# Performance work log

Measured on AMD Instinct MI355X. Metric: run time of the kernel, lower is better.

The kernel has to match this reference:

```python
import jax, jax.numpy as jnp
import numpy as np
from jax import lax

D_MODEL=1024; D_STATE=128; D_CONV=4; EXPAND=2; HEADDIM=64
D_INNER=EXPAND*D_MODEL; NHEADS=D_INNER//HEADDIM
POOL=64; SUMDIM=256; TAU1=0.5; TAU2=0.4

def rmsnorm(x, w, eps):
    return x * lax.rsqrt(jnp.mean(x*x, axis=-1, keepdims=True) + eps) * w

def silu(x):
    return x * jax.nn.sigmoid(x)

def setup_inputs():
    key = jax.random.key(0)
    ks = jax.random.split(key, 20)
    B, T = 4, 2048
    d_in_proj = 2*D_INNER + 2*D_STATE + NHEADS
    inp = {
        'x': jax.random.normal(ks[0], (B, T, D_MODEL), jnp.float32),
        'pool': jnp.zeros((B, POOL, SUMDIM), jnp.float32),
        'priorities': jnp.zeros((B, POOL), jnp.float32),
        'counts': jnp.zeros((B,), jnp.int32),
        'norm_w': jnp.ones((D_MODEL,), jnp.float32),
        'in_w': jax.random.normal(ks[1], (d_in_proj, D_MODEL), jnp.float32)*0.02,
        'conv_w': jax.random.normal(ks[2], (D_INNER+2*D_STATE, 1, D_CONV), jnp.float32)*0.1,
        'conv_b': jnp.zeros((D_INNER+2*D_STATE,), jnp.float32),
        'dt_bias': jax.random.uniform(ks[3], (NHEADS,), jnp.float32, -5.0, -1.0),
        'A_log': jnp.log(jax.random.uniform(ks[4], (NHEADS,), jnp.float32, 1.0, 16.0)),
        'Dp': jax.random.normal(ks[5], (NHEADS,), jnp.float32)*0.1 + 1.0,
        'ssm_norm_w': jnp.ones((D_INNER,), jnp.float32),
        'out_w': jax.random.normal(ks[6], (D_MODEL, D_INNER), jnp.float32)*0.02,
        'score_w1': jax.random.normal(ks[7], (D_MODEL//4, D_MODEL), jnp.float32)*0.03,
        'score_w2': jax.random.normal(ks[8], (1, D_MODEL//4), jnp.float32)*0.06,
        'summ_w': jax.random.normal(ks[9], (SUMDIM, D_MODEL), jnp.float32)*0.03,
        'q_w': jax.random.normal(ks[10], (SUMDIM, D_MODEL), jnp.float32)*0.03,
        'k_w': jax.random.normal(ks[11], (SUMDIM, SUMDIM), jnp.float32)*0.06,
        'v_w': jax.random.normal(ks[12], (D_MODEL, SUMDIM), jnp.float32)*0.06,
        'gate_w': jax.random.normal(ks[13], (D_MODEL, 2*D_MODEL), jnp.float32)*0.02,
    }
    return inp

def mamba2(u, in_w, conv_w, conv_b, dt_bias, A_log, Dp, ssm_norm_w, out_w):
    B, T, _ = u.shape
    zxbcdt = u @ in_w.T                      # [B,T,2*d_inner+2*d_state+nheads]
    z = zxbcdt[..., :D_INNER]
    xBC = zxbcdt[..., D_INNER:2*D_INNER+2*D_STATE]
    dt = jax.nn.softplus(zxbcdt[..., 2*D_INNER+2*D_STATE:] + dt_bias)  # [B,T,H]
    # causal depthwise conv over time
    xc = jnp.transpose(xBC, (0, 2, 1))       # [B,C,T]
    xc = lax.conv_general_dilated(xc, conv_w, (1,), [(D_CONV-1, 0)],
                                  dimension_numbers=('NCH', 'OIH', 'NCH'),
                                  feature_group_count=D_INNER+2*D_STATE)
    xBC = silu(jnp.transpose(xc + conv_b[None, :, None], (0, 2, 1)))
    xh = xBC[..., :D_INNER].reshape(B, T, NHEADS, HEADDIM)
    Bm = xBC[..., D_INNER:D_INNER+D_STATE]   # [B,T,N]
    Cm = xBC[..., D_INNER+D_STATE:]          # [B,T,N]
    A = -jnp.exp(A_log)                      # [H]
    dA = jnp.exp(dt * A)                     # [B,T,H]
    def step(h, inp):
        dA_t, dt_t, x_t, B_t, C_t = inp      # [B,H],[B,H],[B,H,P],[B,N],[B,N]
        h = dA_t[:, :, None, None]*h + (dt_t[:, :, None]*x_t)[..., None]*B_t[:, None, None, :]
        y = jnp.einsum('bhpn,bn->bhp', h, C_t)
        return h, y
    h0 = jnp.zeros((B, NHEADS, HEADDIM, D_STATE), u.dtype)
    xs = (jnp.swapaxes(dA, 0, 1), jnp.swapaxes(dt, 0, 1), jnp.swapaxes(xh, 0, 1),
          jnp.swapaxes(Bm, 0, 1), jnp.swapaxes(Cm, 0, 1))
    _, ys = lax.scan(step, h0, xs)           # [T,B,H,P]
    y = jnp.swapaxes(ys, 0, 1) + Dp[None, None, :, None]*xh
    y = y.reshape(B, T, D_INNER)
    y = rmsnorm(y * silu(z), ssm_norm_w, 1e-5)
    return y @ out_w.T

def pool_update(tokens, scores, pool, priorities, counts,
                summ_w):
    B, T, D = tokens.shape
    mask = scores > TAU1
    order = jnp.argsort(-scores, axis=1)     # descending
    s_scores = jnp.take_along_axis(scores, order, 1)
    s_tokens = jnp.take_along_axis(tokens, order[..., None], 1)
    s_mask = jnp.take_along_axis(mask, order, 1)
    summaries = s_tokens @ summ_w.T          # [B,T,SUMDIM]
    nslots = min(T, POOL)
    bidx = jnp.arange(B)
    def slot_step(carry, inp):
        pool, pri, counts = carry
        has_imp, imp, summ = inp             # [B],[B],[B,SUMDIM]
        add = has_imp & (counts < POOL)
        widx = jnp.minimum(counts, POOL-1)
        pool = pool.at[bidx, widx].set(jnp.where(add[:, None], summ, pool[bidx, widx]))
        pri = pri.at[bidx, widx].set(jnp.where(add, imp, pri[bidx, widx]))
        counts = counts + add.astype(counts.dtype)
        replace = has_imp & (counts >= POOL)
        min_idx = jnp.argmin(pri, axis=1)
        min_p = pri[bidx, min_idx]
        should = replace & (imp > min_p)
        pool = pool.at[bidx, min_idx].set(jnp.where(should[:, None], summ, pool[bidx, min_idx]))
        pri = pri.at[bidx, min_idx].set(jnp.where(should, imp, pri[bidx, min_idx]))
        return (pool, pri, counts), None
    xs = (jnp.swapaxes(s_mask[:, :nslots], 0, 1),
          jnp.swapaxes(s_scores[:, :nslots], 0, 1),
          jnp.swapaxes(summaries[:, :nslots], 0, 1))
    (pool, priorities, counts), _ = lax.scan(slot_step, (pool, priorities, counts), xs)
    return pool, priorities, counts

def reference(x, pool, priorities, counts, norm_w, in_w, conv_w, conv_b, dt_bias,
              A_log, Dp, ssm_norm_w, out_w, score_w1, score_w2, summ_w,
              q_w, k_w, v_w, gate_w):
    B = x.shape[0]
    y = x + mamba2(rmsnorm(x, norm_w, 1e-4), in_w, conv_w, conv_b, dt_bias,
                   A_log, Dp, ssm_norm_w, out_w)
    scores = jax.nn.sigmoid(jnp.maximum(y @ score_w1.T, 0.0) @ score_w2.T)[..., 0]
    # layer_idx % cross_layer_frequency == 0 -> update path taken
    pool, priorities, counts = pool_update(y, scores, pool, priorities, counts, summ_w)
    mask = jnp.arange(POOL)[None, :] < counts[:, None]
    q = y @ q_w.T                            # [B,T,S]
    k = pool @ k_w.T                         # [B,P,S]
    v = pool @ v_w.T                         # [B,P,D]
    attn = jnp.einsum('bts,bps->btp', q, k) / (SUMDIM ** 0.5)
    attn = jnp.where(mask[:, None, :], attn, -jnp.inf)
    attn = jnp.nan_to_num(jax.nn.softmax(attn, axis=-1), nan=0.0)
    retrieved = jnp.einsum('btp,bpd->btd', attn, v)
    gate = jax.nn.sigmoid(jnp.concatenate([y, retrieved], axis=-1) @ gate_w.T)
    rmask = ((jnp.mean(scores, axis=1) > TAU2) & (counts > 0)).astype(y.dtype)[:, None, None]
    y = y + gate * retrieved * rmask
    return (y, pool, priorities, counts)
```

## Files before the change

### kernel.cpp

```cpp
#include <hip/hip_runtime.h>


using u16 = unsigned short;
using bf16x8 = __attribute__((ext_vector_type(8))) short;
using f32x4  = __attribute__((ext_vector_type(4))) float;

#define DEV __device__ __forceinline__

#define GLOAD4(g, l)  __builtin_amdgcn_global_load_lds((const __attribute__((address_space(1))) void*)(g), (__attribute__((address_space(3))) void*)(l), 4, 0, 0)
#define GLOAD16(g, l) __builtin_amdgcn_global_load_lds((const __attribute__((address_space(1))) void*)(g), (__attribute__((address_space(3))) void*)(l), 16, 0, 0)
#define VMWAIT(N) asm volatile("s_waitcnt vmcnt(" #N ")" ::: "memory")

static constexpr int Bb = 4, T = 2048, D = 1024;
static constexpr int DIN = 2048, DST = 128, NH = 32;
static constexpr int DPROJ = 4384;
static constexpr int CCH = 2304;
static constexpr int ROWS = Bb * T;
static constexpr int NC = 4, CL = 512;

DEV float bf2f(u16 h) { union { unsigned int u; float f; } v; v.u = ((unsigned int)h) << 16; return v.f; }
DEV u16 f2bf(float f) { union { float f; unsigned int u; } v; v.f = f; unsigned int r = v.u + 0x7fffu + ((v.u >> 16) & 1u); return (u16)(r >> 16); }
DEV double sigd(double x) { return 1.0 / (1.0 + exp(-x)); }

__global__ void diag_kernel(float* o, float v) { if (threadIdx.x == 0) o[0] = v; }
__global__ void zerod_kernel(double* p, int n) { if ((int)threadIdx.x < n) p[threadIdx.x] = 0.0; }

__global__ void split3_kernel(const float* __restrict__ in, u16* __restrict__ out, long n) {
    long i = (long)blockIdx.x * 256 + threadIdx.x;
    if (i >= n) return;
    float v = in[i];
    u16 h = f2bf(v);
    float r1 = v - bf2f(h);
    u16 m = f2bf(r1);
    out[i] = h;
    out[n + i] = m;
    out[2 * n + i] = f2bf(r1 - bf2f(m));
}

__global__ __launch_bounds__(256) void rms_x_kernel(const float* __restrict__ x, const float* __restrict__ w,
                                                    u16* __restrict__ up, long pstride) {
    long row = blockIdx.x; int tid = threadIdx.x;
    const float* xr = x + row * D;
    float4 xv = *(const float4*)(xr + tid * 4);
    double ss = (double)xv.x * xv.x + (double)xv.y * xv.y + (double)xv.z * xv.z + (double)xv.w * xv.w;
    for (int off = 1; off < 64; off <<= 1) ss += __shfl_xor(ss, off);
    __shared__ double tmp[4];
    if ((tid & 63) == 0) tmp[tid >> 6] = ss;
    __syncthreads();
    double tot = tmp[0] + tmp[1] + tmp[2] + tmp[3];
    double scale = 1.0 / sqrt(tot / (double)D + 1e-4);
    float4 wv = *(const float4*)(w + tid * 4);
    long base = row * D + tid * 4;
    float vals[4];
    vals[0] = (float)((double)xv.x * scale * (double)wv.x);
    vals[1] = (float)((double)xv.y * scale * (double)wv.y);
    vals[2] = (float)((double)xv.z * scale * (double)wv.z);
    vals[3] = (float)((double)xv.w * scale * (double)wv.w);
#pragma unroll
    for (int j = 0; j < 4; j++) {
        float f = vals[j];
        u16 h = f2bf(f);
        float r1 = f - bf2f(h);
        u16 m = f2bf(r1);
        up[base + j] = h;
        up[pstride + base + j] = m;
        up[2 * pstride + base + j] = f2bf(r1 - bf2f(m));
    }
}

template <int NP>
DEV void stage_one(u16* s0, u16* s1, u16* s2, const float* __restrict__ src, long ld,
                   int row0, int lastrow, int k0, int tid) {
    int r = tid >> 1, c0 = (tid & 1) << 4;
    long rg = row0 + r; if (rg > lastrow) rg = lastrow;
    const float* p = src + rg * ld + k0 + c0;
    int base = r * 32 + c0;
    u16 h16[16], m16[16], l16[16];
#pragma unroll
    for (int q = 0; q < 4; q++) {
        float4 v4 = *(const float4*)(p + q * 4);
        float vv[4] = { v4.x, v4.y, v4.z, v4.w };
#pragma unroll
        for (int j = 0; j < 4; j++) {
            float xv = vv[j];
            u16 h = f2bf(xv);
            h16[q * 4 + j] = h;
            if constexpr (NP == 3) {
                float r1 = xv - bf2f(h);
                u16 m = f2bf(r1);
                m16[q * 4 + j] = m;
                l16[q * 4 + j] = f2bf(r1 - bf2f(m));
            }
        }
    }
    *(uint4*)(s0 + base)     = *(const uint4*)(h16);
    *(uint4*)(s0 + base + 8) = *(const uint4*)(h16 + 8);
    if constexpr (NP == 3) {
        *(uint4*)(s1 + base)     = *(const uint4*)(m16);
        *(uint4*)(s1 + base + 8) = *(const uint4*)(m16 + 8);
        *(uint4*)(s2 + base)     = *(const uint4*)(l16);
        *(uint4*)(s2 + base + 8) = *(const uint4*)(l16 + 8);
    }
}

DEV void stage_pre_dma(u16* dst, const u16* __restrict__ src, long ld,
                       int row0, int lastrow, int k0, int wid, int lane) {
#pragma unroll
    for (int j = 0; j < 2; j++) {
        int chunk = wid * 128 + j * 64 + lane;
        int r = chunk >> 2, cs = chunk & 3;
        long rg = row0 + r; if (rg > lastrow) rg = lastrow;
        const u16* g = src + rg * ld + k0 + cs * 8;
        GLOAD16(g, dst + (wid * 128 + j * 64) * 8);
    }
}

template <int NP, int MODE, bool BP, bool AP>
__global__ __launch_bounds__(256) void gemm_f32(
    const float* __restrict__ A, long lda,
    const u16* __restrict__ Ap, size_t astride,
    const float* __restrict__ B, long ldb,
    const u16* __restrict__ Bp, size_t bstride,
    int M, int N, int K,
    float* __restrict__ out0, float* __restrict__ out1,
    const float* __restrict__ aux0, const float* __restrict__ aux1,
    float* __restrict__ dtb, float* __restrict__ dab) {
    __shared__ __align__(16) u16 sm[NP * 2 * 4096];
    u16* As[3]; u16* Bs[3];
#pragma unroll
    for (int p = 0; p < NP; p++) { As[p] = sm + p * 4096; Bs[p] = sm + (NP + p) * 4096; }
    int tid = threadIdx.x, lane = tid & 63, wid = tid >> 6;
    int wr = wid >> 1, wc = wid & 1;
    int nwg = gridDim.x * gridDim.y;
    int wg = blockIdx.y * gridDim.x + blockIdx.x;
    int lin = (wg & 7) * (nwg >> 3) + (wg >> 3);
    int tM = (lin / gridDim.x) * 128, tN = (lin % gridDim.x) * 128;

    f32x4 acc[4][4];
#pragma unroll
    for (int i = 0; i < 4; i++)
#pragma unroll
        for (int j = 0; j < 4; j++) acc[i][j] = f32x4{0.f, 0.f, 0.f, 0.f};

    int nsteps = K / 32;
    for (int kt = 0; kt < nsteps; ++kt) {
        int k0 = kt * 32;
        __syncthreads();
        if constexpr (BP) {
#pragma unroll
            for (int p = 0; p < NP; p++)
                stage_pre_dma(Bs[p], Bp + (size_t)p * bstride, K, tN, N - 1, k0, wid, lane);
        }
        if constexpr (AP) {
#pragma unroll
            for (int p = 0; p < NP; p++)
                stage_pre_dma(As[p], Ap + (size_t)p * astride, K, tM, M - 1, k0, wid, lane);
        } else {
            stage_one<NP>(As[0], NP == 3 ? As[1] : nullptr, NP == 3 ? As[2] : nullptr, A, lda, tM, M - 1, k0, tid);
        }
        if constexpr (!BP) {
            stage_one<NP>(Bs[0], NP == 3 ? Bs[1] : nullptr, NP == 3 ? Bs[2] : nullptr, B, ldb, tN, N - 1, k0, tid);
        }
        __syncthreads();
        int rA = wr * 64 + (lane & 15);
        int rB = wc * 64 + (lane & 15);
        int kk = (lane >> 4) * 8;
        bf16x8 af[NP][4], bfr[NP][4];
#pragma unroll
        for (int p = 0; p < NP; p++)
#pragma unroll
            for (int i = 0; i < 4; i++) {
                af[p][i]  = *(const bf16x8*)(As[p] + (rA + i * 16) * 32 + kk);
                bfr[p][i] = *(const bf16x8*)(Bs[p] + (rB + i * 16) * 32 + kk);
            }
#pragma unroll
        for (int mi = 0; mi < 4; mi++)
#pragma unroll
            for (int ni = 0; ni < 4; ni++) {
                acc[mi][ni] = __builtin_amdgcn_mfma_f32_16x16x32_bf16(af[0][mi], bfr[0][ni], acc[mi][ni], 0, 0, 0);
                if constexpr (NP == 3) {
                    acc[mi][ni] = __builtin_amdgcn_mfma_f32_16x16x32_bf16(af[0][mi], bfr[1][ni], acc[mi][ni], 0, 0, 0);
                    acc[mi][ni] = __builtin_amdgcn_mfma_f32_16x16x32_bf16(af[1][mi], bfr[0][ni], acc[mi][ni], 0, 0, 0);
                    acc[mi][ni] = __builtin_amdgcn_mfma_f32_16x16x32_bf16(af[0][mi], bfr[2][ni], acc[mi][ni], 0, 0, 0);
                    acc[mi][ni] = __builtin_amdgcn_mfma_f32_16x16x32_bf16(af[1][mi], bfr[1][ni], acc[mi][ni], 0, 0, 0);
                    acc[mi][ni] = __builtin_amdgcn_mfma_f32_16x16x32_bf16(af[2][mi], bfr[0][ni], acc[mi][ni], 0, 0, 0);
                }
            }
    }
    int laneh = lane >> 4, lanel = lane & 15;
#pragma unroll
    for (int mi = 0; mi < 4; mi++)
#pragma unroll
        for (int ni = 0; ni < 4; ni++) {
            int col = tN + wc * 64 + ni * 16 + lanel;
            if (col >= N) continue;
#pragma unroll
            for (int r = 0; r < 4; r++) {
                long row = tM + wr * 64 + mi * 16 + laneh * 4 + r;
                float v = acc[mi][ni][r];
                if constexpr (MODE == 0) {
                    if (col < 2048) out0[row * 2048 + col] = v;
                    else if (col < 4352) out1[row * 2304 + (col - 2048)] = v;
                    else {
                        int h = col - 4352;
                        double xx = (double)v + (double)aux0[h];
                        double sp = (xx > 30.0) ? xx : log1p(exp(xx));
                        double a = -exp((double)aux1[h]);
                        dtb[row * NH + h] = (float)sp;
                        dab[row * NH + h] = (float)exp(sp * a);
                    }
                } else if constexpr (MODE == 1) {
                    out0[row * 256 + col] = fmaxf(v, 0.f);
                } else if constexpr (MODE == 2) {
                    float y = aux0[row * 1024 + col] + v;
                    out0[row * 1024 + col] = y;
                    out1[row * 2048 + col] = y;
                } else if constexpr (MODE == 3) {
                    out0[row * 256 + col] = v;
                } else {
                    double g = sigd((double)v);
                    float retr = aux0[row * 2048 + 1024 + col];
                    out0[row * 1024 + col] += (float)(g * (double)retr * (double)aux1[row >> 11]);
                }
            }
        }
}

__global__ __launch_bounds__(256) void conv_kernel(const float* __restrict__ xin, const float* __restrict__ cw,
                                                   const float* __restrict__ cb, float* __restrict__ xbc) {
    int blk = blockIdx.x;
    int ct = blk % 36; int tt = (blk / 36) % 32; int b = blk / (36 * 32);
    int c0 = ct * 64, t0 = tt * 64;
    int tid = threadIdx.x;
    __shared__ float tile[67 * 64];
    for (int i = tid; i < 67 * 64; i += 256) {
        int r = i >> 6, c = i & 63;
        int t = t0 - 3 + r;
        tile[i] = (t >= 0) ? xin[((long)(b * T + t)) * CCH + c0 + c] : 0.f;
    }
    __syncthreads();
    int c = tid & 63; int rb = (tid >> 6) * 16;
    int gc = c0 + c;
    double w0 = cw[gc * 4], w1 = cw[gc * 4 + 1], w2 = cw[gc * 4 + 2], w3 = cw[gc * 4 + 3];
    double bias = cb[gc];
    for (int j = 0; j < 16; j++) {
        int tl = rb + j;
        double a = bias + w0 * (double)tile[tl * 64 + c] + w1 * (double)tile[(tl + 1) * 64 + c]
                        + w2 * (double)tile[(tl + 2) * 64 + c] + w3 * (double)tile[(tl + 3) * 64 + c];
        xbc[((long)(b * T + t0 + tl)) * CCH + gc] = (float)(a * sigd(a));
    }
}

#define SCAN_STEP(tt) do { \
    int slot_ = (tt) & 7; \
    float dtv_ = sdt[(tt)], dav_ = sda[(tt)]; \
    float xt0_ = sx[slot_][pp], xt1_ = sx[slot_][pp + 8]; \
    float dtx0_ = dtv_ * xt0_, dtx1_ = dtv_ * xt1_; \
    const float4* BP_ = (const float4*)&sbc[slot_][0]; \
    float y0a_ = 0.f, y0b_ = 0.f, y1a_ = 0.f, y1b_ = 0.f; \
    _Pragma("unroll") \
    for (int r_ = 0; r_ < 4; r_++) { \
        float4 bv_ = BP_[r_ * 8 + sub]; \
        float4 cv_ = BP_[32 + r_ * 8 + sub]; \
        hs0[r_*4+0] = fmaf(dav_, hs0[r_*4+0], dtx0_ * bv_.x); y0a_ = fmaf(hs0[r_*4+0], cv_.x, y0a_); \
        hs0[r_*4+1] = fmaf(dav_, hs0[r_*4+1], dtx0_ * bv_.y); y0b_ = fmaf(hs0[r_*4+1], cv_.y, y0b_); \
        hs0[r_*4+2] = fmaf(dav_, hs0[r_*4+2], dtx0_ * bv_.z); y0a_ = fmaf(hs0[r_*4+2], cv_.z, y0a_); \
        hs0[r_*4+3] = fmaf(dav_, hs0[r_*4+3], dtx0_ * bv_.w); y0b_ = fmaf(hs0[r_*4+3], cv_.w, y0b_); \
        hs1[r_*4+0] = fmaf(dav_, hs1[r_*4+0], dtx1_ * bv_.x); y1a_ = fmaf(hs1[r_*4+0], cv_.x, y1a_); \
        hs1[r_*4+1] = fmaf(dav_, hs1[r_*4+1], dtx1_ * bv_.y); y1b_ = fmaf(hs1[r_*4+1], cv_.y, y1b_); \
        hs1[r_*4+2] = fmaf(dav_, hs1[r_*4+2], dtx1_ * bv_.z); y1a_ = fmaf(hs1[r_*4+2], cv_.z, y1a_); \
        hs1[r_*4+3] = fmaf(dav_, hs1[r_*4+3], dtx1_ * bv_.w); y1b_ = fmaf(hs1[r_*4+3], cv_.w, y1b_); \
    } \
    float y0_ = y0a_ + y0b_, y1_ = y1a_ + y1b_; \
    y0_ += __shfl_xor(y0_, 1); y0_ += __shfl_xor(y0_, 2); y0_ += __shfl_xor(y0_, 4); \
    y1_ += __shfl_xor(y1_, 1); y1_ += __shfl_xor(y1_, 2); y1_ += __shfl_xor(y1_, 4); \
    if (sub == 0) { \
        yout[(long)(tt) * DIN] = y0_ + sDp * xt0_; \
        yout[(long)(tt) * DIN + 8] = y1_ + sDp * xt1_; \
    } \
    runA *= dav_; \
    if (wrc && l == 0) cumAp[(tt)] = runA; \
} while (0)

#define SCAN_ISSUE(s) do { \
    GLOAD16(bcsrc + (long)(s) * CCH, &sbc[(s) & 7][0]); \
    GLOAD4(xsrc + (long)(s) * CCH, &sx[(s) & 7][0]); \
} while (0)

__global__ __launch_bounds__(64) void scan_kernel(const float* __restrict__ xbc, const float* __restrict__ dtb,
                                                  const float* __restrict__ dab, const float* __restrict__ Dp,
                                                  float* __restrict__ ys, float* __restrict__ hend,
                                                  float* __restrict__ cumA) {
    int bx = blockIdx.x;
    int b = bx >> 9, h = (bx >> 4) & 31, c = (bx >> 2) & 3, q4 = bx & 3;
    int l = threadIdx.x;
    int sub = l & 7, pp = l >> 3;
    __shared__ __align__(16) float sbc[8][256];
    __shared__ __align__(16) float sx[8][64];
    __shared__ float sdt[CL];
    __shared__ float sda[CL];
    long rowc = (long)b * T + (long)c * CL;
    const float* bcrow = xbc + rowc * CCH + 2048;
    const float* xrow  = xbc + rowc * CCH + h * 64 + q4 * 16;
    float* yout = ys + rowc * DIN + h * 64 + q4 * 16 + pp;

    int perm = ((l >> 3) & 3) | ((l & 7) << 2) | (l & 32);
    const float* bcsrc = bcrow + perm * 4;
    const float* xsrc  = xrow + (l & 15);

    bool wrc = (q4 == 0);
    float* cumAp = cumA + ((long)(b * 32 + h)) * T + (long)c * CL;
    float runA = 1.f;

    for (int i = 0; i < CL / 64; i++) {
        GLOAD4(dtb + (rowc + i * 64 + l) * NH + h, &sdt[i * 64]);
        GLOAD4(dab + (rowc + i * 64 + l) * NH + h, &sda[i * 64]);
    }
#pragma unroll
    for (int s = 0; s < 6; s++) SCAN_ISSUE(s);

    float hs0[16], hs1[16];
#pragma unroll
    for (int j = 0; j < 16; j++) { hs0[j] = 0.f; hs1[j] = 0.f; }
    float sDp = Dp[h];

    constexpr int NI = CL / 2;
    for (int i = 0; i < NI - 3; i++) {
        int s0 = 2 * i + 6;
        SCAN_ISSUE(s0);
        SCAN_ISSUE(s0 + 1);
        VMWAIT(12);
        __builtin_amdgcn_sched_barrier(0);
        SCAN_STEP(2 * i);
        SCAN_STEP(2 * i + 1);
    }
    { int i = NI - 3; VMWAIT(8); __builtin_amdgcn_sched_barrier(0); SCAN_STEP(2 * i); SCAN_STEP(2 * i + 1); }
    { int i = NI - 2; VMWAIT(4); __builtin_amdgcn_sched_barrier(0); SCAN_STEP(2 * i); SCAN_STEP(2 * i + 1); }
    { int i = NI - 1; VMWAIT(0); __builtin_amdgcn_sched_barrier(0); SCAN_STEP(2 * i); SCAN_STEP(2 * i + 1); }

    if (c < NC - 1) {
        float* hp = hend + (((long)(b * 32 + h)) * (NC - 1) + c) * 8192 + (q4 * 16 + pp) * 128 + sub * 16;
#pragma unroll
        for (int j = 0; j < 16; j += 4) *(float4*)(hp + j) = *(float4*)&hs0[j];
        float* hp1 = hp + 8 * 128;
#pragma unroll
        for (int j = 0; j < 16; j += 4) *(float4*)(hp1 + j) = *(float4*)&hs1[j];
    }
}

__global__ __launch_bounds__(256) void scanfix_kernel(float* __restrict__ hend, const float* __restrict__ cumA) {
    int bh = blockIdx.x; int tid = threadIdx.x;
    float P1 = cumA[(long)bh * T + 2 * CL - 1];
    float P2 = cumA[(long)bh * T + 3 * CL - 1];
    float* h0 = hend + (long)bh * (NC - 1) * 8192;
    float* h1 = h0 + 8192;
    float* h2 = h1 + 8192;
    for (int e = tid; e < 8192; e += 256) {
        float a = h0[e];
        float b2 = fmaf(P1, a, h1[e]); h1[e] = b2;
        h2[e] = fmaf(P2, b2, h2[e]);
    }
}

__global__ __launch_bounds__(256) void scancorr_kernel(const float* __restrict__ hend, const float* __restrict__ cumA,
                                                       const float* __restrict__ xbc, float* __restrict__ ys) {
    int blk = blockIdx.x;
    int tq = blk & 3;
    int cm = (blk >> 2) % 3;
    int bh = blk / 12;
    int b = bh >> 5, h = bh & 31;
    int tid = threadIdx.x;
    int p = tid >> 2, nq = tid & 3;
    const float* Hin = hend + ((long)bh * (NC - 1) + cm) * 8192 + p * 128 + nq * 32;
    float hreg[32];
#pragma unroll
    for (int j = 0; j < 32; j += 4) *(float4*)&hreg[j] = *(const float4*)(Hin + j);
    __shared__ float sC[8][128];
    long t0 = (long)(cm + 1) * CL + tq * 128;
    const float* cA = cumA + (long)bh * T;
    for (int tg = 0; tg < 16; tg++) {
        __syncthreads();
        {
            int tt = tg * 8 + (tid >> 5);
            int cc = (tid & 31) * 4;
            *(float4*)&sC[tid >> 5][cc] = *(const float4*)(xbc + ((long)b * T + t0 + tt) * CCH + 2176 + cc);
        }
        __syncthreads();
#pragma unroll
        for (int j = 0; j < 8; j++) {
            long t = t0 + tg * 8 + j;
            const float* Cr = &sC[j][nq * 32];
            float d = 0.f;
#pragma unroll
            for (int k = 0; k < 32; k += 4) {
                float4 cv = *(const float4*)(Cr + k);
                d += hreg[k] * cv.x + hreg[k + 1] * cv.y + hreg[k + 2] * cv.z + hreg[k + 3] * cv.w;
            }
            d += __shfl_xor(d, 1);
            d += __shfl_xor(d, 2);
            if (nq == 0) {
                float ca = cA[t];
                ys[((long)b * T + t) * DIN + h * 64 + p] += ca * d;
            }
        }
    }
}

__global__ __launch_bounds__(256) void ssmnorm_kernel(float* __restrict__ ys, const float* __restrict__ z,
                                                      const float* __restrict__ w) {
    long row = blockIdx.x; int tid = threadIdx.x;
    float* yr = ys + row * DIN;
    const float* zr = z + row * DIN;
    double v[8]; double ss = 0.0;
#pragma unroll
    for (int j = 0; j < 8; j++) {
        int c = tid * 8 + j;
        double zz = (double)zr[c];
        double val = (double)yr[c] * (zz * sigd(zz));
        v[j] = val; ss += val * val;
    }
    for (int off = 1; off < 64; off <<= 1) ss += __shfl_xor(ss, off);
    __shared__ double tmp[4];
    if ((tid & 63) == 0) tmp[tid >> 6] = ss;
    __syncthreads();
    double tot = tmp[0] + tmp[1] + tmp[2] + tmp[3];
    double scale = 1.0 / sqrt(tot / (double)DIN + 1e-5);
#pragma unroll
    for (int j = 0; j < 8; j++) {
        int c = tid * 8 + j;
        yr[c] = (float)(v[j] * scale * (double)w[c]);
    }
}

__global__ void score2_kernel(const float* __restrict__ sh, const float* __restrict__ w2,
                              float* __restrict__ scores, double* __restrict__ ssum) {
    int row = blockIdx.x * 4 + (threadIdx.x >> 6);
    int lane = threadIdx.x & 63;
    const float* h = sh + (long)row * 256;
    double a = 0.0;
    for (int j = 0; j < 4; j++) a += (double)h[lane * 4 + j] * (double)w2[lane * 4 + j];
    for (int off = 1; off < 64; off <<= 1) a += __shfl_xor(a, off);
    if (lane == 0) {
        double sc = sigd(a);
        scores[row] = (float)sc;
        atomicAdd(&ssum[row >> 11], sc);
    }
}

__global__ void top64_kernel(const float* __restrict__ scores, int* __restrict__ tidx, float* __restrict__ tval) {
    int b = blockIdx.x; int tid = threadIdx.x;
    __shared__ float s[T];
    __shared__ float rv[256];
    __shared__ int ri[256];
    for (int i = tid; i < T; i += 256) s[i] = scores[b * T + i];
    for (int k = 0; k < 64; k++) {
        __syncthreads();
        float best = -1e30f; int bi = 1 << 30;
        for (int i = tid; i < T; i += 256) {
            float v = s[i];
            if (v > best || (v == best && i < bi)) { best = v; bi = i; }
        }
        rv[tid] = best; ri[tid] = bi;
        __syncthreads();
        for (int off = 128; off > 0; off >>= 1) {
            if (tid < off) {
                float v2 = rv[tid + off]; int i2 = ri[tid + off];
                if (v2 > rv[tid] || (v2 == rv[tid] && i2 < ri[tid])) { rv[tid] = v2; ri[tid] = i2; }
            }
            __syncthreads();
        }
        if (tid == 0) { tidx[b * 64 + k] = ri[0]; tval[b * 64 + k] = rv[0]; s[ri[0]] = -1e30f; }
    }
}

__global__ __launch_bounds__(256) void summ_kernel(const float* __restrict__ y, const int* __restrict__ tidx,
                                                   const float* __restrict__ wsum, float* __restrict__ summ) {
    int s = blockIdx.x & 63; int b = blockIdx.x >> 6;
    int tid = threadIdx.x;
    __shared__ float yrow[1024];
    int tok = tidx[b * 64 + s];
    long base = ((long)(b * T + tok));
    for (int i = tid; i < 1024; i += 256) yrow[i] = y[base * 1024 + i];
    __syncthreads();
    double acc = 0.0;
    const float* w = wsum + (long)tid * 1024;
    for (int kk = 0; kk < 1024; kk++) acc += (double)yrow[kk] * (double)w[kk];
    summ[((long)(b * 64 + s)) * 256 + tid] = (float)acc;
}

__global__ void pool_kernel(const float* __restrict__ pin, const float* __restrict__ prin,
                            const int* __restrict__ cin, const float* __restrict__ tval,
                            const float* __restrict__ summ, const double* __restrict__ ssum,
                            float* __restrict__ pout, float* __restrict__ prout,
                            float* __restrict__ cout, float* __restrict__ rmask) {
    int b = blockIdx.x; int tid = threadIdx.x;
    __shared__ float spri[64];
    __shared__ int scount, sact, sslot, srep, srslot;
    for (int i = tid; i < 64 * 256; i += 256) pout[(long)b * 16384 + i] = pin[(long)b * 16384 + i];
    if (tid < 64) spri[tid] = prin[b * 64 + tid];
    if (tid == 0) scount = cin[b];
    __syncthreads();
    for (int s = 0; s < 64; s++) {
        float imp = tval[b * 64 + s];
        bool has = imp > 0.5f;
        if (tid == 0) {
            sact = 0;
            if (has && scount < 64) { sslot = scount; spri[scount] = imp; scount++; sact = 1; }
        }
        __syncthreads();
        if (sact) pout[((long)(b * 64 + sslot)) * 256 + tid] = summ[((long)(b * 64 + s)) * 256 + tid];
        if (tid < 64) {
            float v = spri[tid]; int idx = tid;
            for (int off = 1; off < 64; off <<= 1) {
                float v2 = __shfl_xor(v, off); int i2 = __shfl_xor(idx, off);
                if (v2 < v || (v2 == v && i2 < idx)) { v = v2; idx = i2; }
            }
            if (tid == 0) {
                srep = 0;
                if (has && scount >= 64 && imp > v) { srep = 1; srslot = idx; spri[idx] = imp; }
            }
        }
        __syncthreads();
        if (srep) pout[((long)(b * 64 + srslot)) * 256 + tid] = summ[((long)(b * 64 + s)) * 256 + tid];
        __syncthreads();
    }
    if (tid < 64) prout[b * 64 + tid] = spri[tid];
    if (tid == 0) {
        cout[b] = (float)scount;
        double mean = ssum[b] / (double)T;
        rmask[b] = (mean > 0.4 && scount > 0) ? 1.f : 0.f;
    }
}

__global__ __launch_bounds__(256) void kv_kernel(const float* __restrict__ pool, const float* __restrict__ kw,
                                                 const float* __restrict__ vw, float* __restrict__ k,
                                                 float* __restrict__ v) {
    int blk = blockIdx.x; int b = blk >> 6, s = blk & 63; int tid = threadIdx.x;
    __shared__ float pr[256];
    pr[tid] = pool[((long)(b * 64 + s)) * 256 + tid];
    __syncthreads();
    float a = 0.f;
    const float* w = kw + (long)tid * 256;
    for (int j = 0; j < 256; j++) a = fmaf(pr[j], w[j], a);
    k[((long)(b * 64 + s)) * 256 + tid] = a;
    for (int m = 0; m < 4; m++) {
        int o = m * 256 + tid;
        const float* w2 = vw + (long)o * 256;
        float c = 0.f;
        for (int j = 0; j < 256; j++) c = fmaf(pr[j], w2[j], c);
        v[((long)(b * 64 + s)) * 1024 + o] = c;
    }
}

__global__ __launch_bounds__(256) void attn_kernel(const float* __restrict__ q, const float* __restrict__ k,
                                                   const float* __restrict__ v, const float* __restrict__ cout,
                                                   float* __restrict__ concat) {
    long row = blockIdx.x;
    int b = (int)(row >> 11);
    int tid = threadIdx.x;
    int cnt = (int)cout[b];
    __shared__ float qs[256], slog[64], sp[64];
    qs[tid] = q[row * 256 + tid];
    __syncthreads();
    int s = tid >> 2, part = tid & 3;
    const float* kr = k + ((long)(b * 64 + s)) * 256 + part * 64;
    float d = 0.f;
    for (int j = 0; j < 64; j++) d = fmaf(qs[part * 64 + j], kr[j], d);
    d += __shfl_xor(d, 1); d += __shfl_xor(d, 2);
    if (part == 0) slog[s] = d * 0.0625f;
    __syncthreads();
    if (tid < 64) {
        float l = (tid < cnt) ? slog[tid] : -1e30f;
        float m = l;
        for (int off = 1; off < 64; off <<= 1) m = fmaxf(m, __shfl_xor(m, off));
        float e = (tid < cnt) ? expf(l - m) : 0.f;
        float su = e;
        for (int off = 1; off < 64; off <<= 1) su += __shfl_xor(su, off);
        sp[tid] = (cnt > 0) ? e / su : 0.f;
    }
    __syncthreads();
    float acc[4] = {0.f, 0.f, 0.f, 0.f};
    for (int s2 = 0; s2 < cnt; s2++) {
        float p = sp[s2];
        const float* vr = v + ((long)(b * 64 + s2)) * 1024 + tid;
        acc[0] = fmaf(p, vr[0], acc[0]);
        acc[1] = fmaf(p, vr[256], acc[1]);
        acc[2] = fmaf(p, vr[512], acc[2]);
        acc[3] = fmaf(p, vr[768], acc[3]);
    }
    for (int j = 0; j < 4; j++) concat[row * 2048 + 1024 + tid + j * 256] = acc[j];
}

extern "C" void kernel_launch(void* const* d_in, const int* in_sizes, int n_in,
                              void* d_out, int out_size, void* d_ws, size_t ws_size,
                              hipStream_t stream) {
    (void)in_sizes; (void)n_in; (void)out_size;
    const float* x       = (const float*)d_in[0];
    const float* pool_in = (const float*)d_in[1];
    const float* pri_in  = (const float*)d_in[2];
    const int*   cnt_in  = (const int*)d_in[3];
    const float* norm_w  = (const float*)d_in[4];
    const float* in_w    = (const float*)d_in[5];
    const float* conv_w  = (const float*)d_in[6];
    const float* conv_b  = (const float*)d_in[7];
    const float* dt_bias = (const float*)d_in[8];
    const float* A_log   = (const float*)d_in[9];
    const float* Dp      = (const float*)d_in[10];
    const float* ssm_w   = (const float*)d_in[11];
    const float* out_w   = (const float*)d_in[12];
    const float* s_w1    = (const float*)d_in[13];
    const float* s_w2    = (const float*)d_in[14];
    const float* summ_w  = (const float*)d_in[15];
    const float* q_w     = (const float*)d_in[16];
    const float* k_w     = (const float*)d_in[17];
    const float* v_w     = (const float*)d_in[18];
    const float* gate_w  = (const float*)d_in[19];

    float* outy    = (float*)d_out;
    float* outpool = outy + (long)ROWS * D;
    float* outpri  = outpool + Bb * 64 * 256;
    float* outcnt  = outpri + Bb * 64;

    char* ws = (char*)d_ws;
    size_t cur = 0;
    auto alloc = [&](size_t bytes) { size_t o = cur; cur += (bytes + 255) / 256 * 256; return o; };

    size_t pw_in_bytes   = (size_t)3 * DPROJ * 1024 * 2;
    size_t uplanes_bytes = (size_t)3 * ROWS * D * 2;
    size_t ra_bytes = pw_in_bytes + uplanes_bytes;

    size_t o_dt   = alloc((size_t)ROWS * NH * 4);
    size_t o_da   = alloc((size_t)ROWS * NH * 4);
    size_t o_sc   = alloc((size_t)ROWS * 4);
    size_t o_ssum = alloc(64);
    size_t o_rmk  = alloc(64);
    size_t o_tidx = alloc(Bb * 64 * 4);
    size_t o_tval = alloc(Bb * 64 * 4);
    size_t o_summ = alloc((size_t)Bb * 64 * 256 * 4);
    size_t o_k    = alloc((size_t)Bb * 64 * 256 * 4);
    size_t o_v    = alloc((size_t)Bb * 64 * 1024 * 4);
    size_t o_hend = alloc((size_t)128 * (NC - 1) * 8192 * 4);
    size_t o_cumA = alloc((size_t)128 * T * 4);
    size_t o_RA = alloc(ra_bytes);
    size_t o_RB = alloc((size_t)ROWS * DIN * 4);
    size_t o_RC = alloc((size_t)ROWS * CCH * 4);

    if (ws_size < cur) {
        diag_kernel<<<1, 64, 0, stream>>>(outy, 1000.0f + (float)(ws_size >> 20));
        return;
    }

    float* dtb    = (float*)(ws + o_dt);
    float* dab    = (float*)(ws + o_da);
    float* scores = (float*)(ws + o_sc);
    double* ssum  = (double*)(ws + o_ssum);
    float* rmk    = (float*)(ws + o_rmk);
    int*   tidx   = (int*)(ws + o_tidx);
    float* tval   = (float*)(ws + o_tval);
    float* summ   = (float*)(ws + o_summ);
    float* kbuf   = (float*)(ws + o_k);
    float* vbuf   = (float*)(ws + o_v);
    float* hend   = (float*)(ws + o_hend);
    float* cumA   = (float*)(ws + o_cumA);

    u16*  pw_in   = (u16*)(ws + o_RA);
    u16*  uplanes = (u16*)(ws + o_RA + pw_in_bytes);
    float* xbc    = (float*)(ws + o_RA);
    float* concat = (float*)(ws + o_RA);
    float* sch    = (float*)(ws + o_RA + (size_t)ROWS * DIN * 4);
    float* bufZ   = (float*)(ws + o_RB);
    u16*  pw_out  = (u16*)(ws + o_RB);
    u16*  pw_s1   = (u16*)(ws + o_RB + (size_t)16 * 1024 * 1024);
    float* qbuf   = (float*)(ws + o_RB);
    float* bufX   = (float*)(ws + o_RC);
    float* yscan  = (float*)(ws + o_RC);

    zerod_kernel<<<1, 64, 0, stream>>>(ssum, 4);
    {
        long n = (long)DPROJ * 1024;
        split3_kernel<<<(n + 255) / 256, 256, 0, stream>>>(in_w, pw_in, n);
    }
    rms_x_kernel<<<ROWS, 256, 0, stream>>>(x, norm_w, uplanes, (long)ROWS * D);
    gemm_f32<3, 0, true, true><<<dim3(35, 64), 256, 0, stream>>>(
        nullptr, 0, uplanes, (size_t)ROWS * D,
        nullptr, 0, pw_in, (size_t)DPROJ * 1024,
        ROWS, DPROJ, 1024,
        bufZ, bufX, dt_bias, A_log, dtb, dab);
    conv_kernel<<<Bb * 32 * 36, 256, 0, stream>>>(bufX, conv_w, conv_b, xbc);
    scan_kernel<<<Bb * NH * NC * 4, 64, 0, stream>>>(xbc, dtb, dab, Dp, yscan, hend, cumA);
    scanfix_kernel<<<128, 256, 0, stream>>>(hend, cumA);
    scancorr_kernel<<<128 * 3 * 4, 256, 0, stream>>>(hend, cumA, xbc, yscan);
    ssmnorm_kernel<<<ROWS, 256, 0, stream>>>(yscan, bufZ, ssm_w);
    {
        long n = (long)1024 * 2048;
        split3_kernel<<<(n + 255) / 256, 256, 0, stream>>>(out_w, pw_out, n);
        long n2 = (long)256 * 1024;
        split3_kernel<<<(n2 + 255) / 256, 256, 0, stream>>>(s_w1, pw_s1, n2);
    }
    gemm_f32<3, 2, true, false><<<dim3(8, 64), 256, 0, stream>>>(
        yscan, 2048, nullptr, 0,
        nullptr, 0, pw_out, (size_t)1024 * 2048,
        ROWS, 1024, 2048,
        outy, concat, x, nullptr, nullptr, nullptr);
    gemm_f32<3, 1, true, false><<<dim3(2, 64), 256, 0, stream>>>(
        outy, 1024, nullptr, 0,
        nullptr, 0, pw_s1, (size_t)256 * 1024,
        ROWS, 256, 1024,
        sch, nullptr, nullptr, nullptr, nullptr, nullptr);
    score2_kernel<<<ROWS / 4, 256, 0, stream>>>(sch, s_w2, scores, ssum);
    top64_kernel<<<Bb, 256, 0, stream>>>(scores, tidx, tval);
    summ_kernel<<<Bb * 64, 256, 0, stream>>>(outy, tidx, summ_w, summ);
    pool_kernel<<<Bb, 256, 0, stream>>>(pool_in, pri_in, cnt_in, tval, summ, ssum,
                                        outpool, outpri, outcnt, rmk);
    kv_kernel<<<Bb * 64, 256, 0, stream>>>(outpool, k_w, v_w, kbuf, vbuf);
    gemm_f32<1, 3, false, false><<<dim3(2, 64), 256, 0, stream>>>(
        outy, 1024, nullptr, 0,
        q_w, 1024, nullptr, 0,
        ROWS, 256, 1024,
        qbuf, nullptr, nullptr, nullptr, nullptr, nullptr);
    attn_kernel<<<ROWS, 256, 0, stream>>>(qbuf, kbuf, vbuf, outcnt, concat);
    gemm_f32<1, 4, false, false><<<dim3(8, 64), 256, 0, stream>>>(
        concat, 2048, nullptr, 0,
        gate_w, 2048, nullptr, 0,
        ROWS, 1024, 2048,
        outy, nullptr, concat, rmk, nullptr, nullptr);
}
```

Baseline: 2.001 ms.

## Replace 3-way bf16 split GEMM emulation with scaled 2-way fp16 split

Switches the fp32-emulating GEMMs from a three-plane bf16 decomposition (six MFMAs per tile step) to a two-plane fp16 hi/lo decomposition with the residual scaled by 4096 (three MFMAs, with separate accumulators). This cuts MFMA work, LDS staging and the planar weight and activation buffers by about a third, and simplifies the split kernels. It trades some accuracy and fp16 range: values beyond the fp16 range or with tiny residuals may lose precision compared with the bf16 triple split.

```diff
diff --git a/kernel.cpp b/kernel.cpp
--- a/kernel.cpp
+++ b/kernel.cpp
@@ -2,7 +2,7 @@
 
 
 using u16 = unsigned short;
-using bf16x8 = __attribute__((ext_vector_type(8))) short;
+using f16x8 = __attribute__((ext_vector_type(8))) _Float16;
 using f32x4  = __attribute__((ext_vector_type(4))) float;
 
 #define DEV __device__ __forceinline__
@@ -17,24 +17,23 @@
 static constexpr int CCH = 2304;
 static constexpr int ROWS = Bb * T;
 static constexpr int NC = 4, CL = 512;
-
-DEV float bf2f(u16 h) { union { unsigned int u; float f; } v; v.u = ((unsigned int)h) << 16; return v.f; }
-DEV u16 f2bf(float f) { union { float f; unsigned int u; } v; v.f = f; unsigned int r = v.u + 0x7fffu + ((v.u >> 16) & 1u); return (u16)(r >> 16); }
+static constexpr float RSC = 4096.f, RSCI = 1.f / 4096.f;
+
+DEV u16 f2h_bits(float f) { union { _Float16 h; u16 u; } v; v.h = (_Float16)f; return v.u; }
+DEV float h2f(u16 u) { union { _Float16 h; u16 u; } v; v.u = u; return (float)v.h; }
 DEV double sigd(double x) { return 1.0 / (1.0 + exp(-x)); }
 
 __global__ void diag_kernel(float* o, float v) { if (threadIdx.x == 0) o[0] = v; }
 __global__ void zerod_kernel(double* p, int n) { if ((int)threadIdx.x < n) p[threadIdx.x] = 0.0; }
 
-__global__ void split3_kernel(const float* __restrict__ in, u16* __restrict__ out, long n) {
+__global__ void split2_kernel(const float* __restrict__ in, u16* __restrict__ out, long n) {
     long i = (long)blockIdx.x * 256 + threadIdx.x;
     if (i >= n) return;
     float v = in[i];
-    u16 h = f2bf(v);
-    float r1 = v - bf2f(h);
-    u16 m = f2bf(r1);
+    u16 h = f2h_bits(v);
+    float r1 = (v - h2f(h)) * RSC;
     out[i] = h;
-    out[n + i] = m;
-    out[2 * n + i] = f2bf(r1 - bf2f(m));
+    out[n + i] = f2h_bits(r1);
 }
 
 __global__ __launch_bounds__(256) void rms_x_kernel(const float* __restrict__ x, const float* __restrict__ w,
@@ -59,23 +58,20 @@
 #pragma unroll
     for (int j = 0; j < 4; j++) {
         float f = vals[j];
-        u16 h = f2bf(f);
-        float r1 = f - bf2f(h);
-        u16 m = f2bf(r1);
+        u16 h = f2h_bits(f);
         up[base + j] = h;
-        up[pstride + base + j] = m;
-        up[2 * pstride + base + j] = f2bf(r1 - bf2f(m));
+        up[pstride + base + j] = f2h_bits((f - h2f(h)) * RSC);
     }
 }
 
 template <int NP>
-DEV void stage_one(u16* s0, u16* s1, u16* s2, const float* __restrict__ src, long ld,
+DEV void stage_one(u16* s0, u16* s1, const float* __restrict__ src, long ld,
                    int row0, int lastrow, int k0, int tid) {
     int r = tid >> 1, c0 = (tid & 1) << 4;
     long rg = row0 + r; if (rg > lastrow) rg = lastrow;
     const float* p = src + rg * ld + k0 + c0;
     int base = r * 32 + c0;
-    u16 h16[16], m16[16], l16[16];
+    u16 h16[16], l16[16];
 #pragma unroll
     for (int q = 0; q < 4; q++) {
         float4 v4 = *(const float4*)(p + q * 4);
@@ -83,23 +79,16 @@
 #pragma unroll
         for (int j = 0; j < 4; j++) {
             float xv = vv[j];
-            u16 h = f2bf(xv);
+            u16 h = f2h_bits(xv);
             h16[q * 4 + j] = h;
-            if constexpr (NP == 3) {
-                float r1 = xv - bf2f(h);
-                u16 m = f2bf(r1);
-                m16[q * 4 + j] = m;
-                l16[q * 4 + j] = f2bf(r1 - bf2f(m));
-            }
+            if constexpr (NP == 2) l16[q * 4 + j] = f2h_bits((xv - h2f(h)) * RSC);
         }
     }
     *(uint4*)(s0 + base)     = *(const uint4*)(h16);
     *(uint4*)(s0 + base + 8) = *(const uint4*)(h16 + 8);
-    if constexpr (NP == 3) {
-        *(uint4*)(s1 + base)     = *(const uint4*)(m16);
-        *(uint4*)(s1 + base + 8) = *(const uint4*)(m16 + 8);
-        *(uint4*)(s2 + base)     = *(const uint4*)(l16);
-        *(uint4*)(s2 + base + 8) = *(const uint4*)(l16 + 8);
+    if constexpr (NP == 2) {
+        *(uint4*)(s1 + base)     = *(const uint4*)(l16);
+        *(uint4*)(s1 + base + 8) = *(const uint4*)(l16 + 8);
     }
 }
 
@@ -126,7 +115,7 @@
     const float* __restrict__ aux0, const float* __restrict__ aux1,
     float* __restrict__ dtb, float* __restrict__ dab) {
     __shared__ __align__(16) u16 sm[NP * 2 * 4096];
-    u16* As[3]; u16* Bs[3];
+    u16* As[2]; u16* Bs[2];
 #pragma unroll
     for (int p = 0; p < NP; p++) { As[p] = sm + p * 4096; Bs[p] = sm + (NP + p) * 4096; }
     int tid = threadIdx.x, lane = tid & 63, wid = tid >> 6;
@@ -136,11 +125,14 @@
     int lin = (wg & 7) * (nwg >> 3) + (wg >> 3);
     int tM = (lin / gridDim.x) * 128, tN = (lin % gridDim.x) * 128;
 
-    f32x4 acc[4][4];
+    f32x4 acc1[4][4], acc2[4][4];
 #pragma unroll
     for (int i = 0; i < 4; i++)
 #pragma unroll
-        for (int j = 0; j < 4; j++) acc[i][j] = f32x4{0.f, 0.f, 0.f, 0.f};
+        for (int j = 0; j < 4; j++) {
+            acc1[i][j] = f32x4{0.f, 0.f, 0.f, 0.f};
+            if constexpr (NP == 2) acc2[i][j] = f32x4{0.f, 0.f, 0.f, 0.f};
+        }
 
     int nsteps = K / 32;
     for (int kt = 0; kt < nsteps; ++kt) {
@@ -156,34 +148,31 @@
             for (int p = 0; p < NP; p++)
                 stage_pre_dma(As[p], Ap + (size_t)p * astride, K, tM, M - 1, k0, wid, lane);
         } else {
-            stage_one<NP>(As[0], NP == 3 ? As[1] : nullptr, NP == 3 ? As[2] : nullptr, A, lda, tM, M - 1, k0, tid);
+            stage_one<NP>(As[0], NP == 2 ? As[1] : nullptr, A, lda, tM, M - 1, k0, tid);
         }
         if constexpr (!BP) {
-            stage_one<NP>(Bs[0], NP == 3 ? Bs[1] : nullptr, NP == 3 ? Bs[2] : nullptr, B, ldb, tN, N - 1, k0, tid);
+            stage_one<NP>(Bs[0], NP == 2 ? Bs[1] : nullptr, B, ldb, tN, N - 1, k0, tid);
         }
         __syncthreads();
         int rA = wr * 64 + (lane & 15);
         int rB = wc * 64 + (lane & 15);
         int kk = (lane >> 4) * 8;
-        bf16x8 af[NP][4], bfr[NP][4];
+        f16x8 af[NP][4], bfr[NP][4];
 #pragma unroll
         for (int p = 0; p < NP; p++)
 #pragma unroll
             for (int i = 0; i < 4; i++) {
-                af[p][i]  = *(const bf16x8*)(As[p] + (rA + i * 16) * 32 + kk);
-                bfr[p][i] = *(const bf16x8*)(Bs[p] + (rB + i * 16) * 32 + kk);
+                af[p][i]  = *(const f16x8*)(As[p] + (rA + i * 16) * 32 + kk);
+                bfr[p][i] = *(const f16x8*)(Bs[p] + (rB + i * 16) * 32 + kk);
             }
 #pragma unroll
         for (int mi = 0; mi < 4; mi++)
 #pragma unroll
             for (int ni = 0; ni < 4; ni++) {
-                acc[mi][ni] = __builtin_amdgcn_mfma_f32_16x16x32_bf16(af[0][mi], bfr[0][ni], acc[mi][ni], 0, 0, 0);
-                if constexpr (NP == 3) {
-                    acc[mi][ni] = __builtin_amdgcn_mfma_f32_16x16x32_bf16(af[0][mi], bfr[1][ni], acc[mi][ni], 0, 0, 0);
-                    acc[mi][ni] = __builtin_amdgcn_mfma_f32_16x16x32_bf16(af[1][mi], bfr[0][ni], acc[mi][ni], 0, 0, 0);
-                    acc[mi][ni] = __builtin_amdgcn_mfma_f32_16x16x32_bf16(af[0][mi], bfr[2][ni], acc[mi][ni], 0, 0, 0);
-                    acc[mi][ni] = __builtin_amdgcn_mfma_f32_16x16x32_bf16(af[1][mi], bfr[1][ni], acc[mi][ni], 0, 0, 0);
-                    acc[mi][ni] = __builtin_amdgcn_mfma_f32_16x16x32_bf16(af[2][mi], bfr[0][ni], acc[mi][ni], 0, 0, 0);
+                acc1[mi][ni] = __builtin_amdgcn_mfma_f32_16x16x32_f16(af[0][mi], bfr[0][ni], acc1[mi][ni], 0, 0, 0);
+                if constexpr (NP == 2) {
+                    acc2[mi][ni] = __builtin_amdgcn_mfma_f32_16x16x32_f16(af[0][mi], bfr[1][ni], acc2[mi][ni], 0, 0, 0);
+                    acc2[mi][ni] = __builtin_amdgcn_mfma_f32_16x16x32_f16(af[1][mi], bfr[0][ni], acc2[mi][ni], 0, 0, 0);
                 }
             }
     }
@@ -197,7 +186,8 @@
 #pragma unroll
             for (int r = 0; r < 4; r++) {
                 long row = tM + wr * 64 + mi * 16 + laneh * 4 + r;
-                float v = acc[mi][ni][r];
+                float v = acc1[mi][ni][r];
+                if constexpr (NP == 2) v += acc2[mi][ni][r] * RSCI;
                 if constexpr (MODE == 0) {
                     if (col < 2048) out0[row * 2048 + col] = v;
                     else if (col < 4352) out1[row * 2304 + (col - 2048)] = v;
@@ -625,9 +615,9 @@
     size_t cur = 0;
     auto alloc = [&](size_t bytes) { size_t o = cur; cur += (bytes + 255) / 256 * 256; return o; };
 
-    size_t pw_in_bytes   = (size_t)3 * DPROJ * 1024 * 2;
-    size_t uplanes_bytes = (size_t)3 * ROWS * D * 2;
-    size_t ra_bytes = pw_in_bytes + uplanes_bytes;
+    size_t pw_in_bytes   = (size_t)2 * DPROJ * 1024 * 2;
+    size_t uplanes_bytes = (size_t)2 * ROWS * D * 2;
+    size_t ra_bytes = (size_t)ROWS * CCH * 4;
 
     size_t o_dt   = alloc((size_t)ROWS * NH * 4);
     size_t o_da   = alloc((size_t)ROWS * NH * 4);
@@ -678,10 +668,10 @@
     zerod_kernel<<<1, 64, 0, stream>>>(ssum, 4);
     {
         long n = (long)DPROJ * 1024;
-        split3_kernel<<<(n + 255) / 256, 256, 0, stream>>>(in_w, pw_in, n);
+        split2_kernel<<<(n + 255) / 256, 256, 0, stream>>>(in_w, pw_in, n);
     }
     rms_x_kernel<<<ROWS, 256, 0, stream>>>(x, norm_w, uplanes, (long)ROWS * D);
-    gemm_f32<3, 0, true, true><<<dim3(35, 64), 256, 0, stream>>>(
+    gemm_f32<2, 0, true, true><<<dim3(35, 64), 256, 0, stream>>>(
         nullptr, 0, uplanes, (size_t)ROWS * D,
         nullptr, 0, pw_in, (size_t)DPROJ * 1024,
         ROWS, DPROJ, 1024,
@@ -693,16 +683,16 @@
     ssmnorm_kernel<<<ROWS, 256, 0, stream>>>(yscan, bufZ, ssm_w);
     {
         long n = (long)1024 * 2048;
-        split3_kernel<<<(n + 255) / 256, 256, 0, stream>>>(out_w, pw_out, n);
+        split2_kernel<<<(n + 255) / 256, 256, 0, stream>>>(out_w, pw_out, n);
         long n2 = (long)256 * 1024;
-        split3_kernel<<<(n2 + 255) / 256, 256, 0, stream>>>(s_w1, pw_s1, n2);
-    }
-    gemm_f32<3, 2, true, false><<<dim3(8, 64), 256, 0, stream>>>(
+        split2_kernel<<<(n2 + 255) / 256, 256, 0, stream>>>(s_w1, pw_s1, n2);
+    }
+    gemm_f32<2, 2, true, false><<<dim3(8, 64), 256, 0, stream>>>(
         yscan, 2048, nullptr, 0,
         nullptr, 0, pw_out, (size_t)1024 * 2048,
         ROWS, 1024, 2048,
         outy, concat, x, nullptr, nullptr, nullptr);
-    gemm_f32<3, 1, true, false><<<dim3(2, 64), 256, 0, stream>>>(
+    gemm_f32<2, 1, true, false><<<dim3(2, 64), 256, 0, stream>>>(
         outy, 1024, nullptr, 0,
         nullptr, 0, pw_s1, (size_t)256 * 1024,
         ROWS, 256, 1024,
```

Result: slower. 2.070 ms (+3.5%).
